# Optimization experiments

Hardware: AMD Instinct MI355X
Metric: run time of the kernel (lower is better)

## Reference

```python
import jax, jax.numpy as jnp
import numpy as np

D_MODEL = 2048
N_Q_HEADS = 32
N_KV_HEADS = 8
HEAD_DIM = D_MODEL // N_Q_HEADS  # 64
KV_DIM = HEAD_DIM * N_KV_HEADS   # 512
B, S = 2, 2048


def setup_inputs() -> dict:
    key = jax.random.key(0)
    ks = jax.random.split(key, 11)
    sc_d = 1.0 / np.sqrt(D_MODEL)
    return {
        "query": jax.random.normal(ks[0], (B, S, D_MODEL), jnp.float32),
        "key":   jax.random.normal(ks[1], (B, S, D_MODEL), jnp.float32),
        "value": jax.random.normal(ks[2], (B, S, D_MODEL), jnp.float32),
        "Wq": jax.random.normal(ks[3], (D_MODEL, D_MODEL), jnp.float32) * sc_d,
        "bq": jnp.zeros((D_MODEL,), jnp.float32),
        "Wk": jax.random.normal(ks[4], (D_MODEL, KV_DIM), jnp.float32) * sc_d,
        "bk": jnp.zeros((KV_DIM,), jnp.float32),
        "Wv": jax.random.normal(ks[5], (D_MODEL, KV_DIM), jnp.float32) * sc_d,
        "bv": jnp.zeros((KV_DIM,), jnp.float32),
        "Wo": jax.random.normal(ks[6], (D_MODEL, D_MODEL), jnp.float32) * sc_d,
        "bo": jnp.zeros((D_MODEL,), jnp.float32),
    }


def reference(query, key, value, Wq, bq, Wk, bk, Wv, bv, Wo, bo):
    b, s, _ = query.shape
    g = N_Q_HEADS // N_KV_HEADS  # num groups
    # projections
    Q = query @ Wq + bq                      # [b, s, d_model]
    K = key @ Wk + bk                        # [b, s, kv_dim]
    V = value @ Wv + bv                      # [b, s, kv_dim]
    # split heads. Torch code splits Q into groups of num_kv_heads heads,
    # and each group broadcasts per-head against the Hkv KV heads, i.e.
    # query head (grp*Hkv + j) attends against kv head j.
    Q = Q.reshape(b, s, g, N_KV_HEADS, HEAD_DIM)  # [b, s, g, hkv, d]
    K = K.reshape(b, s, N_KV_HEADS, HEAD_DIM)     # [b, s, hkv, d]
    V = V.reshape(b, s, N_KV_HEADS, HEAD_DIM)
    scale = 1.0 / jnp.sqrt(jnp.float32(HEAD_DIM))
    scores = jnp.einsum('bsghd,bthd->bghst', Q, K) * scale  # [b,g,hkv,s,s]
    attn = jax.nn.softmax(scores, axis=-1)
    out = jnp.einsum('bghst,bthd->bsghd', attn, V)          # [b,s,g,hkv,d]
    # concat over groups then heads == original head order (g major, hkv minor)
    out = out.reshape(b, s, D_MODEL)
    return out @ Wo + bo
```

## Files before the change

### kernel.cpp

```cpp
#include <hip/hip_runtime.h>
#include <cstdint>

typedef _Float16 half4 __attribute__((ext_vector_type(4)));
typedef _Float16 half8 __attribute__((ext_vector_type(8)));
typedef _Float16 half16 __attribute__((ext_vector_type(16)));
typedef float f32x4 __attribute__((ext_vector_type(4)));
typedef float f32x16 __attribute__((ext_vector_type(16)));

#define L2E 1.44269504088896340736f

__device__ __forceinline__ void gl16(const void* g, void* l) {
  __builtin_amdgcn_global_load_lds(
      (const __attribute__((address_space(1))) void*)g,
      (__attribute__((address_space(3))) void*)l, 16, 0, 0);
}

__device__ __forceinline__ uint32_t pk2(float a, float b) {
  return __builtin_bit_cast(uint32_t, __builtin_amdgcn_cvt_pkrtz(a, b));
}

__device__ __forceinline__ void plswap(uint32_t& x, uint32_t& y) {
  auto r = __builtin_amdgcn_permlane32_swap((int)x, (int)y, false, false);
  x = (uint32_t)r[0];
  y = (uint32_t)r[1];
}

__device__ __forceinline__ f32x16 zero16() {
  f32x16 z;
  #pragma unroll
  for (int r = 0; r < 16; ++r) z[r] = 0.0f;
  return z;
}

__global__ __launch_bounds__(256) void cvt_f32_f16_3(
    const float* __restrict__ s0, const float* __restrict__ s1, const float* __restrict__ s2,
    _Float16* __restrict__ d0, _Float16* __restrict__ d1, _Float16* __restrict__ d2)
{
  const float* src = (blockIdx.z == 0) ? s0 : (blockIdx.z == 1 ? s1 : s2);
  _Float16* dst    = (blockIdx.z == 0) ? d0 : (blockIdx.z == 1 ? d1 : d2);
  size_t i = ((size_t)blockIdx.x * 256 + threadIdx.x) * 8;
  float4 a = *(const float4*)(src + i);
  float4 b = *(const float4*)(src + i + 4);
  half8 o;
  o[0] = (_Float16)a.x; o[1] = (_Float16)a.y; o[2] = (_Float16)a.z; o[3] = (_Float16)a.w;
  o[4] = (_Float16)b.x; o[5] = (_Float16)b.y; o[6] = (_Float16)b.z; o[7] = (_Float16)b.w;
  *(half8*)(dst + i) = o;
}

__global__ __launch_bounds__(256) void transpose_w(
    const float* __restrict__ src, _Float16* __restrict__ dst, const int N, const int K)
{
  __shared__ float t[32][33];
  const int n0 = blockIdx.x * 32, k0 = blockIdx.y * 32;
  #pragma unroll
  for (int i = 0; i < 4; ++i)
    t[threadIdx.y + i * 8][threadIdx.x] =
        src[(size_t)(k0 + threadIdx.y + i * 8) * N + n0 + threadIdx.x];
  __syncthreads();
  #pragma unroll
  for (int i = 0; i < 4; ++i)
    dst[(size_t)(n0 + threadIdx.y + i * 8) * K + k0 + threadIdx.x] =
        (_Float16)t[threadIdx.x][threadIdx.y + i * 8];
}

__global__ __launch_bounds__(256) void transpose_v(
    const _Float16* __restrict__ QKV, _Float16* __restrict__ VT)
{
  const int bh = blockIdx.z;
  const int bb = bh >> 3, h = bh & 7;
  const int t0 = blockIdx.x * 32, d0 = blockIdx.y * 32;
  __shared__ _Float16 t[32][33];
  const _Float16* src = QKV + (size_t)(bb * 2048) * 3072 + 2560 + h * 64;
  #pragma unroll
  for (int i = 0; i < 4; ++i)
    t[threadIdx.y + i * 8][threadIdx.x] =
        src[(size_t)(t0 + threadIdx.y + i * 8) * 3072 + d0 + threadIdx.x];
  __syncthreads();
  _Float16* dst = VT + ((size_t)(bb * 8 + h) * 64) * 2048;
  #pragma unroll
  for (int i = 0; i < 4; ++i)
    dst[(size_t)(d0 + threadIdx.y + i * 8) * 2048 + t0 + threadIdx.x] =
        t[threadIdx.x][threadIdx.y + i * 8];
}

template<int MODE>
__global__ __launch_bounds__(256) void gemm_f16(
    const _Float16* __restrict__ Aq, const _Float16* __restrict__ Ak, const _Float16* __restrict__ Av,
    const _Float16* __restrict__ Bt,
    const float* __restrict__ bias0, const float* __restrict__ bias1, const float* __restrict__ bias2,
    _Float16* __restrict__ Ch, float* __restrict__ Cf, const int K, const int N)
{
  const int m0 = blockIdx.x * 128;
  const int n0 = blockIdx.y * 128;
  const _Float16* A = Aq;
  if constexpr (MODE == 0) { if (n0 >= 2560) A = Av; else if (n0 >= 2048) A = Ak; }
  const int tid = threadIdx.x;
  const int lane = tid & 63;
  const int w = tid >> 6;
  const int wr = w >> 1, wc = w & 1;
  const int lo = lane & 15, hi = lane >> 4;

  __shared__ __align__(1024) _Float16 Asm[128 * 64];
  __shared__ __align__(1024) _Float16 Bsm[128 * 64];

  f32x4 acc[4][4];
  #pragma unroll
  for (int i = 0; i < 4; ++i)
    #pragma unroll
    for (int j = 0; j < 4; ++j)
      acc[i][j] = (f32x4){0.f, 0.f, 0.f, 0.f};

  const int li = lane >> 3;
  const int lc = lane & 7;
  const int kslot = lc ^ li;
  const _Float16* Asrc = A  + (size_t)(m0 + w * 32 + li) * K + kslot * 8;
  const _Float16* Bsrc = Bt + (size_t)(n0 + w * 32 + li) * K + kslot * 8;
  char* Adst = (char*)Asm + w * 4096;
  char* Bdst = (char*)Bsm + w * 4096;

  for (int k0 = 0; k0 < K; k0 += 64) {
    __syncthreads();
    #pragma unroll
    for (int u = 0; u < 4; ++u) {
      gl16(Asrc + k0 + (size_t)u * 8 * K, Adst + u * 1024);
      gl16(Bsrc + k0 + (size_t)u * 8 * K, Bdst + u * 1024);
    }
    __syncthreads();
    #pragma unroll
    for (int kp = 0; kp < 2; ++kp) {
      half8 af[4], bf[4];
      #pragma unroll
      for (int i = 0; i < 4; ++i) {
        const int ra = wr * 64 + i * 16 + lo;
        af[i] = *(const half8*)((const char*)Asm + ra * 128 + ((kp * 64 + hi * 16) ^ ((ra & 7) << 4)));
        const int rb = wc * 64 + i * 16 + lo;
        bf[i] = *(const half8*)((const char*)Bsm + rb * 128 + ((kp * 64 + hi * 16) ^ ((rb & 7) << 4)));
      }
      #pragma unroll
      for (int i = 0; i < 4; ++i)
        #pragma unroll
        for (int j = 0; j < 4; ++j)
          acc[i][j] = __builtin_amdgcn_mfma_f32_16x16x32_f16(af[i], bf[j], acc[i][j], 0, 0, 0);
    }
  }

  float* T = (float*)Asm;
  const int tr = tid >> 3;
  const int slot = tid & 7;
  #pragma unroll
  for (int i = 0; i < 4; ++i) {
    __syncthreads();
    #pragma unroll
    for (int j = 0; j < 4; ++j)
      #pragma unroll
      for (int r = 0; r < 4; ++r)
        T[(wr * 16 + 4 * hi + r) * 128 + wc * 64 + j * 16 + lo] = acc[i][j][r];
    __syncthreads();
    const int grow = m0 + (tr >> 4) * 64 + i * 16 + (tr & 15);
    const int gcol = n0 + slot * 16;
    const float* Trow = T + tr * 128 + slot * 16;
    float4 v[4];
    #pragma unroll
    for (int q = 0; q < 4; ++q) v[q] = ((const float4*)Trow)[q];
    const float* bp = bias0;
    int cb = gcol;
    if constexpr (MODE == 0) {
      if (gcol >= 2560) { bp = bias2; cb = gcol - 2560; }
      else if (gcol >= 2048) { bp = bias1; cb = gcol - 2048; }
    }
    float4 bvv[4];
    #pragma unroll
    for (int q = 0; q < 4; ++q) bvv[q] = ((const float4*)(bp + cb))[q];
    if constexpr (MODE == 0) {
      half16 o;
      #pragma unroll
      for (int q = 0; q < 4; ++q) {
        o[4 * q + 0] = (_Float16)(v[q].x + bvv[q].x);
        o[4 * q + 1] = (_Float16)(v[q].y + bvv[q].y);
        o[4 * q + 2] = (_Float16)(v[q].z + bvv[q].z);
        o[4 * q + 3] = (_Float16)(v[q].w + bvv[q].w);
      }
      *(half16*)(Ch + (size_t)grow * N + gcol) = o;
    } else {
      float* dst = Cf + (size_t)grow * N + gcol;
      #pragma unroll
      for (int q = 0; q < 4; ++q) {
        float4 ov = {v[q].x + bvv[q].x, v[q].y + bvv[q].y, v[q].z + bvv[q].z, v[q].w + bvv[q].w};
        ((float4*)dst)[q] = ov;
      }
    }
  }
}

__global__ __launch_bounds__(256, 2) void attn_fwd2(
    const _Float16* __restrict__ QKV, const _Float16* __restrict__ VT,
    _Float16* __restrict__ AO)
{
  const int wg = blockIdx.x;
  const int work = (wg & 7) * 64 + (wg >> 3);
  const int bh = work >> 5;
  const int b = bh >> 3, h = bh & 7;
  const int rem = work & 31;
  const int qh = (rem >> 3) * 8 + h;
  const int qt = rem & 7;

  const int tid = threadIdx.x;
  const int lane = tid & 63;
  const int w = tid >> 6;
  const int l31 = lane & 31;
  const int hi5 = lane >> 5;
  const int r7 = l31 & 7;

  __shared__ __align__(1024) char sm[2][2][8192];

  const float SCALE = 0.125f * L2E;

  const int qrow0 = b * 2048 + qt * 256 + w * 64 + l31;
  half8 qf[2][4];
  #pragma unroll
  for (int qb = 0; qb < 2; ++qb) {
    const _Float16* qp = QKV + (size_t)(qrow0 + qb * 32) * 3072 + qh * 64 + hi5 * 8;
    #pragma unroll
    for (int s = 0; s < 4; ++s)
      qf[qb][s] = *(const half8*)(qp + s * 16);
  }

  const int li = lane >> 3;
  const int lc = lane & 7;
  const int kslot = lc ^ li;
  const int w16li = w * 16 + li;
  const _Float16* Ksrc = QKV + ((size_t)(b * 2048 + w16li)) * 3072 + 2048 + h * 64 + kslot * 8;
  const _Float16* Vsrc = VT + ((size_t)(b * 8 + h) * 64 + w16li) * 2048 + kslot * 8;

  f32x16 oa[2][2];
  #pragma unroll
  for (int i = 0; i < 2; ++i)
    #pragma unroll
    for (int qb = 0; qb < 2; ++qb) oa[i][qb] = zero16();
  float mreg[2] = {-3.0e38f, -3.0e38f};
  float lreg[2] = {0.f, 0.f};

  {
    char* kd = &sm[0][0][0] + w * 2048;
    char* vd = &sm[0][1][0] + w * 2048;
    gl16(Ksrc, kd);
    gl16(Ksrc + (size_t)8 * 3072, kd + 1024);
    gl16(Vsrc, vd);
    gl16(Vsrc + (size_t)8 * 2048, vd + 1024);
  }
  __syncthreads();

  int cur = 0;
  for (int t = 0; t < 32; ++t) {
    if (t < 31) {
      const int t0 = (t + 1) * 64;
      char* kd = &sm[cur ^ 1][0][0] + w * 2048;
      char* vd = &sm[cur ^ 1][1][0] + w * 2048;
      const _Float16* kg = Ksrc + (size_t)t0 * 3072;
      const _Float16* vg = Vsrc + t0;
      gl16(kg, kd);
      gl16(kg + (size_t)8 * 3072, kd + 1024);
      gl16(vg, vd);
      gl16(vg + (size_t)8 * 2048, vd + 1024);
    }

    const char* Kb = &sm[cur][0][0];
    const char* Vb = &sm[cur][1][0];

    f32x16 sa[2][2];
    #pragma unroll
    for (int j = 0; j < 2; ++j)
      #pragma unroll
      for (int qb = 0; qb < 2; ++qb) sa[j][qb] = zero16();
    #pragma unroll
    for (int s = 0; s < 4; ++s) {
      #pragma unroll
      for (int j = 0; j < 2; ++j) {
        const int kr = j * 32 + l31;
        half8 kf = *(const half8*)(Kb + kr * 128 + (((2 * s + hi5) ^ r7) << 4));
        sa[j][0] = __builtin_amdgcn_mfma_f32_32x32x16_f16(kf, qf[0][s], sa[j][0], 0, 0, 0);
        sa[j][1] = __builtin_amdgcn_mfma_f32_32x32x16_f16(kf, qf[1][s], sa[j][1], 0, 0, 0);
      }
    }

    #pragma unroll
    for (int qb = 0; qb < 2; ++qb) {
      float pm = -3.0e38f;
      #pragma unroll
      for (int j = 0; j < 2; ++j)
        #pragma unroll
        for (int r = 0; r < 16; ++r) {
          const float v = sa[j][qb][r] * SCALE;
          sa[j][qb][r] = v;
          pm = fmaxf(pm, v);
        }
      pm = fmaxf(pm, __shfl_xor(pm, 32));
      const float mnew = fmaxf(mreg[qb], pm);
      const float corr = __builtin_amdgcn_exp2f(mreg[qb] - mnew);
      mreg[qb] = mnew;
      float ps = 0.f;
      #pragma unroll
      for (int j = 0; j < 2; ++j)
        #pragma unroll
        for (int r = 0; r < 16; ++r) {
          const float p = __builtin_amdgcn_exp2f(sa[j][qb][r] - mnew);
          sa[j][qb][r] = p;
          ps += p;
        }
      ps += __shfl_xor(ps, 32);
      lreg[qb] = lreg[qb] * corr + ps;
      #pragma unroll
      for (int i = 0; i < 2; ++i)
        #pragma unroll
        for (int r = 0; r < 16; ++r)
          oa[i][qb][r] *= corr;
    }

    uint32_t pw[2][4][4];
    #pragma unroll
    for (int qb = 0; qb < 2; ++qb)
      #pragma unroll
      for (int j = 0; j < 2; ++j)
        #pragma unroll
        for (int hf = 0; hf < 2; ++hf) {
          const int rb = hf * 8;
          uint32_t w0 = pk2(sa[j][qb][rb + 0], sa[j][qb][rb + 1]);
          uint32_t w1 = pk2(sa[j][qb][rb + 2], sa[j][qb][rb + 3]);
          uint32_t w2 = pk2(sa[j][qb][rb + 4], sa[j][qb][rb + 5]);
          uint32_t w3 = pk2(sa[j][qb][rb + 6], sa[j][qb][rb + 7]);
          plswap(w0, w2);
          plswap(w1, w3);
          const int s = 2 * j + hf;
          pw[qb][s][0] = w0; pw[qb][s][1] = w1; pw[qb][s][2] = w2; pw[qb][s][3] = w3;
        }

    #pragma unroll
    for (int s = 0; s < 4; ++s) {
      union { uint32_t u[4]; half8 h; } p0, p1;
      #pragma unroll
      for (int u = 0; u < 4; ++u) { p0.u[u] = pw[0][s][u]; p1.u[u] = pw[1][s][u]; }
      #pragma unroll
      for (int i = 0; i < 2; ++i) {
        const int vr = i * 32 + l31;
        half8 vf = *(const half8*)(Vb + vr * 128 + (((2 * s + hi5) ^ r7) << 4));
        oa[i][0] = __builtin_amdgcn_mfma_f32_32x32x16_f16(vf, p0.h, oa[i][0], 0, 0, 0);
        oa[i][1] = __builtin_amdgcn_mfma_f32_32x32x16_f16(vf, p1.h, oa[i][1], 0, 0, 0);
      }
    }

    __syncthreads();
    cur ^= 1;
  }

  #pragma unroll
  for (int qb = 0; qb < 2; ++qb) {
    const float inv = 1.0f / lreg[qb];
    const int row = qrow0 + qb * 32;
    #pragma unroll
    for (int i = 0; i < 2; ++i) {
      _Float16* dst = AO + (size_t)row * 2048 + qh * 64 + i * 32 + hi5 * 4;
      #pragma unroll
      for (int q = 0; q < 4; ++q) {
        union { uint32_t u[2]; half4 h4; } o;
        o.u[0] = pk2(oa[i][qb][4 * q + 0] * inv, oa[i][qb][4 * q + 1] * inv);
        o.u[1] = pk2(oa[i][qb][4 * q + 2] * inv, oa[i][qb][4 * q + 3] * inv);
        *(half4*)(dst + 8 * q) = o.h4;
      }
    }
  }
}

extern "C" void kernel_launch(void* const* d_in, const int* in_sizes, int n_in,
                              void* d_out, int out_size, void* d_ws, size_t ws_size,
                              hipStream_t stream) {
  const float* query = (const float*)d_in[0];
  const float* key   = (const float*)d_in[1];
  const float* value = (const float*)d_in[2];
  const float* Wq = (const float*)d_in[3];
  const float* bq = (const float*)d_in[4];
  const float* Wk = (const float*)d_in[5];
  const float* bk = (const float*)d_in[6];
  const float* Wv = (const float*)d_in[7];
  const float* bv = (const float*)d_in[8];
  const float* Wo = (const float*)d_in[9];
  const float* bo = (const float*)d_in[10];
  float* out = (float*)d_out;

  char* ws = (char*)d_ws;
  _Float16* qh    = (_Float16*)(ws);
  _Float16* kh    = (_Float16*)(ws + 16777216);
  _Float16* vh    = (_Float16*)(ws + 33554432);
  _Float16* WqkvT = (_Float16*)(ws + 50331648);
  _Float16* WoT   = (_Float16*)(ws + 62914560);
  _Float16* QKVh  = (_Float16*)(ws + 71303168);
  _Float16* VT    = (_Float16*)(ws + 96468992);
  _Float16* aoh   = (_Float16*)(ws + 100663296);

  cvt_f32_f16_3<<<dim3(4096, 1, 3), 256, 0, stream>>>(query, key, value, qh, kh, vh);
  transpose_w<<<dim3(64, 64), dim3(32, 8), 0, stream>>>(Wq, WqkvT, 2048, 2048);
  transpose_w<<<dim3(16, 64), dim3(32, 8), 0, stream>>>(Wk, WqkvT + (size_t)2048 * 2048, 512, 2048);
  transpose_w<<<dim3(16, 64), dim3(32, 8), 0, stream>>>(Wv, WqkvT + (size_t)2560 * 2048, 512, 2048);
  transpose_w<<<dim3(64, 64), dim3(32, 8), 0, stream>>>(Wo, WoT, 2048, 2048);
  gemm_f16<0><<<dim3(32, 24), 256, 0, stream>>>(qh, kh, vh, WqkvT, bq, bk, bv,
                                                QKVh, nullptr, 2048, 3072);
  transpose_v<<<dim3(64, 2, 16), dim3(32, 8), 0, stream>>>(QKVh, VT);
  attn_fwd2<<<512, 256, 0, stream>>>(QKVh, VT, aoh);
  gemm_f16<1><<<dim3(32, 16), 256, 0, stream>>>(aoh, nullptr, nullptr, WoT, bo,
                                                nullptr, nullptr, nullptr, out, 2048, 2048);
}
```

Before: 281.2 us.

## Merge weight transposes into one launch and add lazy-rescale softmax with MFMA priority

```diff
diff --git a/kernel.cpp b/kernel.cpp
--- a/kernel.cpp
+++ b/kernel.cpp
@@ -47,11 +47,21 @@
   *(half8*)(dst + i) = o;
 }
 
-__global__ __launch_bounds__(256) void transpose_w(
-    const float* __restrict__ src, _Float16* __restrict__ dst, const int N, const int K)
+__global__ __launch_bounds__(256) void transpose_w_all(
+    const float* __restrict__ Wq, const float* __restrict__ Wk,
+    const float* __restrict__ Wv, const float* __restrict__ Wo,
+    _Float16* __restrict__ WqkvT, _Float16* __restrict__ WoT)
 {
+  int id = blockIdx.x;
+  const float* src;
+  _Float16* dst;
+  int N, tx, ty;
+  if (id < 4096)      { src = Wq; dst = WqkvT;                        N = 2048; tx = id & 63; ty = id >> 6; }
+  else if (id < 5120) { id -= 4096; src = Wk; dst = WqkvT + (size_t)2048 * 2048; N = 512; tx = id & 15; ty = id >> 4; }
+  else if (id < 6144) { id -= 5120; src = Wv; dst = WqkvT + (size_t)2560 * 2048; N = 512; tx = id & 15; ty = id >> 4; }
+  else                { id -= 6144; src = Wo; dst = WoT;              N = 2048; tx = id & 63; ty = id >> 6; }
+  const int n0 = tx * 32, k0 = ty * 32;
   __shared__ float t[32][33];
-  const int n0 = blockIdx.x * 32, k0 = blockIdx.y * 32;
   #pragma unroll
   for (int i = 0; i < 4; ++i)
     t[threadIdx.y + i * 8][threadIdx.x] =
@@ -59,7 +69,7 @@
   __syncthreads();
   #pragma unroll
   for (int i = 0; i < 4; ++i)
-    dst[(size_t)(n0 + threadIdx.y + i * 8) * K + k0 + threadIdx.x] =
+    dst[(size_t)(n0 + threadIdx.y + i * 8) * 2048 + k0 + threadIdx.x] =
         (_Float16)t[threadIdx.x][threadIdx.y + i * 8];
 }
 
@@ -192,7 +202,7 @@
   }
 }
 
-__global__ __launch_bounds__(256, 2) void attn_fwd2(
+__global__ __launch_bounds__(256, 2) void attn_fwd3(
     const _Float16* __restrict__ QKV, const _Float16* __restrict__ VT,
     _Float16* __restrict__ AO)
 {
@@ -213,16 +223,18 @@
 
   __shared__ __align__(1024) char sm[2][2][8192];
 
-  const float SCALE = 0.125f * L2E;
-
   const int qrow0 = b * 2048 + qt * 256 + w * 64 + l31;
   half8 qf[2][4];
   #pragma unroll
   for (int qb = 0; qb < 2; ++qb) {
     const _Float16* qp = QKV + (size_t)(qrow0 + qb * 32) * 3072 + qh * 64 + hi5 * 8;
     #pragma unroll
-    for (int s = 0; s < 4; ++s)
-      qf[qb][s] = *(const half8*)(qp + s * 16);
+    for (int s = 0; s < 4; ++s) {
+      half8 q = *(const half8*)(qp + s * 16);
+      #pragma unroll
+      for (int e = 0; e < 8; ++e) q[e] = q[e] * (_Float16)0.125f;
+      qf[qb][s] = q;
+    }
   }
 
   const int li = lane >> 3;
@@ -237,7 +249,8 @@
   for (int i = 0; i < 2; ++i)
     #pragma unroll
     for (int qb = 0; qb < 2; ++qb) oa[i][qb] = zero16();
-  float mreg[2] = {-3.0e38f, -3.0e38f};
+  float mreg[2] = {-1.0e30f, -1.0e30f};
+  float mn2[2]  = {-1.0e30f, -1.0e30f};
   float lreg[2] = {0.f, 0.f};
 
   {
@@ -272,6 +285,7 @@
     for (int j = 0; j < 2; ++j)
       #pragma unroll
       for (int qb = 0; qb < 2; ++qb) sa[j][qb] = zero16();
+    __builtin_amdgcn_s_setprio(1);
     #pragma unroll
     for (int s = 0; s < 4; ++s) {
       #pragma unroll
@@ -282,38 +296,41 @@
         sa[j][1] = __builtin_amdgcn_mfma_f32_32x32x16_f16(kf, qf[1][s], sa[j][1], 0, 0, 0);
       }
     }
+    __builtin_amdgcn_s_setprio(0);
 
     #pragma unroll
     for (int qb = 0; qb < 2; ++qb) {
-      float pm = -3.0e38f;
+      float pm = -1.0e30f;
+      #pragma unroll
+      for (int j = 0; j < 2; ++j)
+        #pragma unroll
+        for (int r = 0; r < 16; ++r)
+          pm = fmaxf(pm, sa[j][qb][r]);
+      pm = fmaxf(pm, __shfl_xor(pm, 32));
+      if (__any(pm - mreg[qb] > 5.5f)) {
+        const float mnew = fmaxf(mreg[qb], pm);
+        const float corr = __builtin_amdgcn_exp2f((mreg[qb] - mnew) * L2E);
+        mreg[qb] = mnew;
+        mn2[qb] = mnew * L2E;
+        lreg[qb] *= corr;
+        #pragma unroll
+        for (int i = 0; i < 2; ++i)
+          #pragma unroll
+          for (int r = 0; r < 16; ++r)
+            oa[i][qb][r] *= corr;
+      }
+      const float nmn2 = -mn2[qb];
+      float ps = 0.f;
       #pragma unroll
       for (int j = 0; j < 2; ++j)
         #pragma unroll
         for (int r = 0; r < 16; ++r) {
-          const float v = sa[j][qb][r] * SCALE;
-          sa[j][qb][r] = v;
-          pm = fmaxf(pm, v);
-        }
-      pm = fmaxf(pm, __shfl_xor(pm, 32));
-      const float mnew = fmaxf(mreg[qb], pm);
-      const float corr = __builtin_amdgcn_exp2f(mreg[qb] - mnew);
-      mreg[qb] = mnew;
-      float ps = 0.f;
-      #pragma unroll
-      for (int j = 0; j < 2; ++j)
-        #pragma unroll
-        for (int r = 0; r < 16; ++r) {
-          const float p = __builtin_amdgcn_exp2f(sa[j][qb][r] - mnew);
+          const float p = __builtin_amdgcn_exp2f(fmaf(sa[j][qb][r], L2E, nmn2));
           sa[j][qb][r] = p;
           ps += p;
         }
       ps += __shfl_xor(ps, 32);
-      lreg[qb] = lreg[qb] * corr + ps;
-      #pragma unroll
-      for (int i = 0; i < 2; ++i)
-        #pragma unroll
-        for (int r = 0; r < 16; ++r)
-          oa[i][qb][r] *= corr;
+      lreg[qb] += ps;
     }
 
     uint32_t pw[2][4][4];
@@ -334,6 +351,7 @@
           pw[qb][s][0] = w0; pw[qb][s][1] = w1; pw[qb][s][2] = w2; pw[qb][s][3] = w3;
         }
 
+    __builtin_amdgcn_s_setprio(1);
     #pragma unroll
     for (int s = 0; s < 4; ++s) {
       union { uint32_t u[4]; half8 h; } p0, p1;
@@ -347,6 +365,7 @@
         oa[i][1] = __builtin_amdgcn_mfma_f32_32x32x16_f16(vf, p1.h, oa[i][1], 0, 0, 0);
       }
     }
+    __builtin_amdgcn_s_setprio(0);
 
     __syncthreads();
     cur ^= 1;
@@ -397,14 +416,11 @@
   _Float16* aoh   = (_Float16*)(ws + 100663296);
 
   cvt_f32_f16_3<<<dim3(4096, 1, 3), 256, 0, stream>>>(query, key, value, qh, kh, vh);
-  transpose_w<<<dim3(64, 64), dim3(32, 8), 0, stream>>>(Wq, WqkvT, 2048, 2048);
-  transpose_w<<<dim3(16, 64), dim3(32, 8), 0, stream>>>(Wk, WqkvT + (size_t)2048 * 2048, 512, 2048);
-  transpose_w<<<dim3(16, 64), dim3(32, 8), 0, stream>>>(Wv, WqkvT + (size_t)2560 * 2048, 512, 2048);
-  transpose_w<<<dim3(64, 64), dim3(32, 8), 0, stream>>>(Wo, WoT, 2048, 2048);
+  transpose_w_all<<<10240, dim3(32, 8), 0, stream>>>(Wq, Wk, Wv, Wo, WqkvT, WoT);
   gemm_f16<0><<<dim3(32, 24), 256, 0, stream>>>(qh, kh, vh, WqkvT, bq, bk, bv,
                                                 QKVh, nullptr, 2048, 3072);
   transpose_v<<<dim3(64, 2, 16), dim3(32, 8), 0, stream>>>(QKVh, VT);
-  attn_fwd2<<<512, 256, 0, stream>>>(QKVh, VT, aoh);
+  attn_fwd3<<<512, 256, 0, stream>>>(QKVh, VT, aoh);
   gemm_f16<1><<<dim3(32, 16), 256, 0, stream>>>(aoh, nullptr, nullptr, WoT, bo,
                                                 nullptr, nullptr, nullptr, out, 2048, 2048);
 }
```

Result: faster. 265.1 us (-5.7%).
